# Optimization experiments

Hardware: AMD Instinct MI355X
Metric: run time of the kernel (lower is better)

Reference implementation:

```python
import jax, jax.numpy as jnp
import numpy as np
from jax import lax

# 19 edges over 19 body-joint heatmap channels (0..18); PAF channels are 19..56
EDGES = np.array([[1,8],[8,9],[9,10],[1,11],[11,12],[12,13],[1,2],[2,3],[3,4],[2,16],
                  [1,5],[5,6],[6,7],[5,17],[0,1],[0,14],[0,15],[14,16],[15,17]], dtype=np.int32)
_i = np.arange(19, dtype=np.int32)
# per-edge 4 input channels: [node_a, node_b, paf_x(=19+2i), paf_y(=20+2i)]
CH_IDX = np.concatenate([EDGES, (19 + 2*_i)[:, None], (20 + 2*_i)[:, None]], axis=1)  # [19,4]

_W_SHAPES = [(16,4,5,5),(16,16,5,5),(32,16,5,5),(32,32,5,5),(32,32,5,5),(128,32,1,1),(2,128,1,1)]

def _conv(x, w, b):
    p = (w.shape[-1] - 1) // 2  # padding=2 for 5x5, 0 for 1x1
    y = lax.conv_general_dilated(x, w, window_strides=(1,1), padding=[(p,p),(p,p)],
                                 dimension_numbers=('NCHW','OIHW','NCHW'))
    return y + b[None, :, None, None]

def setup_inputs() -> dict:
    key = jax.random.key(0)
    keys = jax.random.split(key, 1 + 2*len(_W_SHAPES))
    N, C, H, W = 16, 57, 128, 128
    inp = {'cnn_output': jax.random.normal(keys[0], (N, C, H, W), dtype=jnp.float32),
           'gnn_interations': 1}
    for i, s in enumerate(_W_SHAPES):
        inp[f'w{i}'] = jax.random.normal(keys[1+2*i], s, dtype=jnp.float32) * 0.01
        inp[f'b{i}'] = jax.random.normal(keys[2+2*i], (s[0],), dtype=jnp.float32) * 0.01
    return inp

def reference(cnn_output, gnn_interations, w0, b0, w1, b1, w2, b2, w3, b3, w4, b4, w5, b5, w6, b6):
    N, _, H, Wd = cnn_output.shape
    ws = (w0, w1, w2, w3, w4, w5, w6)
    bs = (b0, b1, b2, b3, b4, b5, b6)
    # gather per-edge 4-channel inputs: [N,19,4,H,W] -> fold edges into batch
    x = cnn_output[:, jnp.asarray(CH_IDX)]            # [N,19,4,H,W]
    x = x.reshape(N * 19, 4, H, Wd)
    for i in range(7):
        x = _conv(x, ws[i], bs[i])
        if i != 6:
            x = jax.nn.relu(x)
    # edge n output (2 ch) -> output channels [2n, 2n+1]
    return x.reshape(N, 38, H, Wd)
```

## Files before the change

kernel.cpp:

```cpp
#include <hip/hip_runtime.h>
#include <hip/hip_bf16.h>

typedef __bf16  bf16x8 __attribute__((ext_vector_type(8)));
typedef float   f32x4  __attribute__((ext_vector_type(4)));
typedef int     i32x4  __attribute__((ext_vector_type(4)));
typedef int     i32x8  __attribute__((ext_vector_type(8)));

__device__ __constant__ int EDGE_A[19] = {1,8,9,1,11,12,1,2,3,2,1,5,6,5,0,0,0,14,15};
__device__ __constant__ int EDGE_B[19] = {8,9,10,11,12,13,2,3,4,16,5,6,7,17,1,14,15,16,17};

#define SACT  64.0f
#define SINV  (1.0f / 4096.0f)
#define SREQ  0.015625f
#define SCL1  0x7F7F7F7F

__device__ __forceinline__ unsigned short f2bf(float f) {
    unsigned int x = __float_as_uint(f);
    x += 0x7FFFu + ((x >> 16) & 1u);
    return (unsigned short)(x >> 16);
}
__device__ __forceinline__ unsigned int pack2(float a, float b) {
    __hip_bfloat162 t = __float22bfloat162_rn(make_float2(a, b));
    unsigned int r; __builtin_memcpy(&r, &t, 4); return r;
}
__device__ __forceinline__ unsigned char f2fp8(float v) {
    int r = __builtin_amdgcn_cvt_pk_fp8_f32(v, 0.f, 0, false);
    return (unsigned char)(r & 0xff);
}
__device__ __forceinline__ unsigned int pk4fp8(float a, float b, float c, float d) {
    int v = __builtin_amdgcn_cvt_pk_fp8_f32(a, b, 0, false);
    v = __builtin_amdgcn_cvt_pk_fp8_f32(c, d, v, true);
    return (unsigned int)v;
}
__device__ __forceinline__ unsigned int quant4(f32x4 a, float4 b, float s, bool oob) {
    float v0 = fmaxf(fmaf(a[0], s, b.x), 0.f);
    float v1 = fmaxf(fmaf(a[1], s, b.y), 0.f);
    float v2 = fmaxf(fmaf(a[2], s, b.z), 0.f);
    float v3 = fmaxf(fmaf(a[3], s, b.w), 0.f);
    unsigned int v = pk4fp8(v0, v1, v2, v3);
    return oob ? 0u : v;
}

__device__ __forceinline__ int sw8 (int l) { return l ^ ((l >> 4) & 8);  }
__device__ __forceinline__ int sw48(int l) { return l ^ ((l >> 3) & 48); }

__device__ __forceinline__ void store_relu4(unsigned char* dst, f32x4 a, float4 b, bool oob) {
    unsigned int lo = pack2(fmaxf(a[0] + b.x, 0.f), fmaxf(a[1] + b.y, 0.f));
    unsigned int hi = pack2(fmaxf(a[2] + b.z, 0.f), fmaxf(a[3] + b.w, 0.f));
    uint2 v; v.x = oob ? 0u : lo; v.y = oob ? 0u : hi;
    *(uint2*)dst = v;
}

extern "C" __global__ void __launch_bounds__(256)
reorder_weights(const float* __restrict__ w0, const float* __restrict__ w1,
                const float* __restrict__ w2, const float* __restrict__ w3,
                const float* __restrict__ w4, const float* __restrict__ w5,
                unsigned char* __restrict__ ws)
{
    int idx = blockIdx.x * 256 + threadIdx.x;
    unsigned short* wsS = (unsigned short*)ws;
    if (idx < 4096) {
        int k = idx & 31, oc = idx >> 5;
        wsS[idx] = f2bf(w5[oc * 32 + k]);
    } else if (idx < 6144) {
        int j = idx - 4096;
        int k = j & 31, n = (j >> 5) & 15, c = j >> 9;
        int t = c * 8 + (k >> 2), ic = k & 3;
        float v = (t < 25) ? w0[(n * 4 + ic) * 25 + t] : 0.f;
        wsS[idx] = f2bf(v);
    }
    if (idx < 6656) {
        int k = idx & 31, n = (idx >> 5) & 15, tp = idx >> 9;
        int t = 2 * tp + (k >> 4), ic = k & 15;
        float v = (t < 25) ? w1[(n * 16 + ic) * 25 + t] * SACT : 0.f;
        ws[12288 + idx] = f2fp8(v);
    } else if (idx < 19968) {
        int j = idx - 6656;
        int k = j & 31, n = (j >> 5) & 15, nt = (j >> 9) & 1, tp = j >> 10;
        int t = 2 * tp + (k >> 4), ic = k & 15, oc = nt * 16 + n;
        float v = (t < 25) ? w2[(oc * 16 + ic) * 25 + t] * SACT : 0.f;
        ws[18944 + j] = f2fp8(v);
    } else if (idx < 48640) {
        int j = idx - 19968;
        int tg = j >> 12, r = j & 4095;
        int nt = r >> 11, n = (r >> 7) & 15, q = (r >> 5) & 3, ic = r & 31;
        int tap = 4 * tg + q;
        float v = (tap < 25) ? w3[((nt * 16 + n) * 32 + ic) * 25 + tap] * SACT : 0.f;
        ws[32256 + j] = f2fp8(v);
    } else if (idx < 77312) {
        int j = idx - 48640;
        int tg = j >> 12, r = j & 4095;
        int nt = r >> 11, n = (r >> 7) & 15, q = (r >> 5) & 3, ic = r & 31;
        int tap = 4 * tg + q;
        float v = (tap < 25) ? w4[((nt * 16 + n) * 32 + ic) * 25 + tap] * SACT : 0.f;
        ws[60928 + j] = f2fp8(v);
    }
}

__device__ __forceinline__ void conv0_slab(
    const unsigned short* __restrict__ s_in, unsigned char* __restrict__ s0,
    const unsigned char* __restrict__ wB, const float* __restrict__ b0,
    int yoff, int oy, int ox, int wave, int lane)
{
    const int nl = lane & 15, quad = lane >> 4;
    const unsigned short* w0p = (const unsigned short*)(wB + 8192);
    bf16x8 wf[4];
#pragma unroll
    for (int c = 0; c < 4; ++c)
        wf[c] = *(const bf16x8*)(w0p + c * 512 + nl * 32 + quad * 8);
    float4 bb = *(const float4*)(b0 + quad * 4);
    float4 bbs = make_float4(bb.x * SACT, bb.y * SACT, bb.z * SACT, bb.w * SACT);

    int coff0[4], coff1[4];
#pragma unroll
    for (int c = 0; c < 4; ++c) {
        int t0 = c * 8 + quad * 2, t1 = t0 + 1;
        if (t0 > 24) t0 = 24;
        if (t1 > 24) t1 = 24;
        coff0[c] = ((t0 / 5) * 36 + (t0 % 5)) * 8;
        coff1[c] = ((t1 / 5) * 36 + (t1 % 5)) * 8;
    }
    const unsigned char* sB = (const unsigned char*)s_in;

#pragma unroll 1
    for (int i = 0; i < 9; ++i) {
        int mt = wave + 4 * i;
        int p = mt * 16 + nl;
        int y = p >> 5, x = p & 31;
        int abase = (y * 36 + x) * 8;
        f32x4 acc = (f32x4)0.f;
#pragma unroll
        for (int c = 0; c < 4; ++c) {
            uint2 lo = *(const uint2*)(sB + abase + coff0[c]);
            uint2 hi = *(const uint2*)(sB + abase + coff1[c]);
            bf16x8 a;
            ((uint2*)&a)[0] = lo; ((uint2*)&a)[1] = hi;
            acc = __builtin_amdgcn_mfma_f32_16x16x32_bf16(wf[c], a, acc, 0, 0, 0);
        }
        bool oob = ((unsigned)(oy - 8 + y + yoff) >= 128u) || ((unsigned)(ox - 8 + x) >= 128u);
        *(unsigned int*)(s0 + sw8(p * 16 + quad * 4)) = quant4(acc, bbs, SACT, oob);
    }
}

__device__ __forceinline__ void conv1_fp8(
    const unsigned char* __restrict__ s0, unsigned char* __restrict__ s1,
    const unsigned char* __restrict__ wB, const float* __restrict__ b1,
    int POFF, int gy0, int gx0, int wave, int lane)
{
    const int nl = lane & 15, quad = lane >> 4;
    const int h = quad >> 1, g8 = (quad & 1) * 8;

    int abase[7];
#pragma unroll
    for (int i = 0; i < 7; ++i) {
        int p = (wave + 4 * i) * 16 + nl;
        if (p > 391) p = 391;
        int y = p / 28, x = p - y * 28;
        abase[i] = (y * 32 + x) * 16 + g8;
    }
    f32x4 acc[7];
#pragma unroll
    for (int i = 0; i < 7; ++i) acc[i] = (f32x4)0.f;

    const unsigned char* wp = wB + 12288 + nl * 32 + quad * 8;

#pragma unroll 1
    for (int c0 = 0; c0 < 13; c0 += 5) {
        long wl[5];
#pragma unroll
        for (int tp = 0; tp < 5; ++tp)
            if (c0 + tp < 13) wl[tp] = *(const long*)(wp + (c0 + tp) * 512);
#pragma unroll
        for (int tp = 0; tp < 5; ++tp) {
            if (c0 + tp < 13) {
                int t = 2 * (c0 + tp) + h;
                if (t > 24) t = 24;
                int dy = t / 5, dx = t - 5 * dy;
                int toff = (dy * 32 + dx) * 16;
#pragma unroll
                for (int i = 0; i < 7; ++i)
                    if (wave + 4 * i < 25) {
                        long a = *(const long*)(s0 + sw8(abase[i] + toff));
                        acc[i] = __builtin_amdgcn_mfma_f32_16x16x32_fp8_fp8(wl[tp], a, acc[i], 0, 0, 0);
                    }
            }
        }
    }

    float4 bb = *(const float4*)(b1 + quad * 4);
    float4 bbs = make_float4(bb.x * SACT, bb.y * SACT, bb.z * SACT, bb.w * SACT);
#pragma unroll
    for (int i = 0; i < 7; ++i) {
        int p = (wave + 4 * i) * 16 + nl;
        if (p < 392) {
            int pg = p + POFF;
            int y = pg / 28, x = pg - y * 28;
            bool oob = ((unsigned)(gy0 + y) >= 128u) || ((unsigned)(gx0 + x) >= 128u);
            *(unsigned int*)(s1 + sw8(pg * 16 + quad * 4)) = quant4(acc[i], bbs, SREQ, oob);
        }
    }
}

template<int I0, int NI>
__device__ __forceinline__ void conv2_fp8(
    const unsigned char* __restrict__ s1, unsigned char* __restrict__ s2,
    const unsigned char* __restrict__ wA, const float* __restrict__ b2,
    int gy0, int gx0, int wave, int lane)
{
    const int nl = lane & 15, quad = lane >> 4;
    const int h = quad >> 1, g8 = (quad & 1) * 8;

    int abase[NI];
#pragma unroll
    for (int i = 0; i < NI; ++i) {
        int p = (wave + 4 * (I0 + i)) * 16 + nl;
        int y = p / 24, x = p - y * 24;
        abase[i] = (y * 28 + x) * 16 + g8;
    }
    f32x4 acc[NI][2];
#pragma unroll
    for (int i = 0; i < NI; ++i) { acc[i][0] = (f32x4)0.f; acc[i][1] = (f32x4)0.f; }

    const unsigned char* wp = wA + nl * 32 + quad * 8;

#pragma unroll 1
    for (int c0 = 0; c0 < 13; c0 += 3) {
        long wl[3][2];
#pragma unroll
        for (int tp = 0; tp < 3; ++tp)
            if (c0 + tp < 13) {
                wl[tp][0] = *(const long*)(wp + ((c0 + tp) * 2 + 0) * 512);
                wl[tp][1] = *(const long*)(wp + ((c0 + tp) * 2 + 1) * 512);
            }
#pragma unroll
        for (int tp = 0; tp < 3; ++tp) {
            if (c0 + tp < 13) {
                int t = 2 * (c0 + tp) + h;
                if (t > 24) t = 24;
                int dy = t / 5, dx = t - 5 * dy;
                int toff = (dy * 28 + dx) * 16;
#pragma unroll
                for (int i = 0; i < NI; ++i) {
                    long a = *(const long*)(s1 + sw8(abase[i] + toff));
                    acc[i][0] = __builtin_amdgcn_mfma_f32_16x16x32_fp8_fp8(wl[tp][0], a, acc[i][0], 0, 0, 0);
                    acc[i][1] = __builtin_amdgcn_mfma_f32_16x16x32_fp8_fp8(wl[tp][1], a, acc[i][1], 0, 0, 0);
                }
            }
        }
    }

#pragma unroll
    for (int i = 0; i < NI; ++i) {
        int p = (wave + 4 * (I0 + i)) * 16 + nl;
        int y = p / 24, x = p - y * 24;
        bool oob = ((unsigned)(gy0 + y) >= 128u) || ((unsigned)(gx0 + x) >= 128u);
#pragma unroll
        for (int nt = 0; nt < 2; ++nt) {
            float4 bb = *(const float4*)(b2 + nt * 16 + quad * 4);
            float4 bbs = make_float4(bb.x * SACT, bb.y * SACT, bb.z * SACT, bb.w * SACT);
            int byte = (p * 32 + nt * 16 + quad * 4) ^ ((p & 4) << 2);
            *(unsigned int*)(s2 + byte) = quant4(acc[i][nt], bbs, SREQ, oob);
        }
    }
}

template<int SINW, int SOUT, int MAXM, bool GUARD, bool FP8OUT, bool INXOR, int INSTRIDE>
__device__ __forceinline__ void conv_c32_mx(
    const unsigned char* __restrict__ sinB, unsigned char* __restrict__ soutB,
    const unsigned char* __restrict__ wA, const float* __restrict__ bias,
    int gy0, int gx0, int wave, int lane)
{
    constexpr int NM = (SOUT * SOUT) / 16;
    const int nl = lane & 15, quad = lane >> 4;

    int abase[MAXM];
#pragma unroll
    for (int i = 0; i < MAXM; ++i) {
        int p = (wave + 4 * i) * 16 + nl;
        if (GUARD && p > SOUT * SOUT - 1) p = SOUT * SOUT - 1;
        int y = p / SOUT, x = p - y * SOUT;
        abase[i] = (y * SINW + x) * INSTRIDE;
    }
    f32x4 acc[MAXM][2];
#pragma unroll
    for (int i = 0; i < MAXM; ++i) { acc[i][0] = (f32x4)0.f; acc[i][1] = (f32x4)0.f; }

    const unsigned char* wp = wA + nl * 128 + quad * 32;

#pragma unroll 1
    for (int tg = 0; tg < 7; ++tg) {
        int t = 4 * tg + quad;
        if (t > 24) t = 24;
        int dy = t / 5, dx = t - 5 * dy;
        int to = (dy * SINW + dx) * INSTRIDE;
        i32x8 wl0 = *(const i32x8*)(wp + tg * 4096);
        i32x8 wl1 = *(const i32x8*)(wp + tg * 4096 + 2048);
#pragma unroll
        for (int i = 0; i < MAXM; ++i)
            if (!GUARD || wave + 4 * i < NM) {
                int ad = abase[i] + to;
                if (INXOR) ad ^= (ad >> 3) & 16;
                i32x4 alo = *(const i32x4*)(sinB + ad);
                i32x4 ahi = *(const i32x4*)(sinB + (INXOR ? (ad ^ 16) : (ad + 16)));
                i32x8 a;
                ((i32x4*)&a)[0] = alo; ((i32x4*)&a)[1] = ahi;
                acc[i][0] = __builtin_amdgcn_mfma_scale_f32_16x16x128_f8f6f4(
                                wl0, a, acc[i][0], 0, 0, 0, SCL1, 0, SCL1);
                acc[i][1] = __builtin_amdgcn_mfma_scale_f32_16x16x128_f8f6f4(
                                wl1, a, acc[i][1], 0, 0, 0, SCL1, 0, SCL1);
            }
    }

#pragma unroll
    for (int i = 0; i < MAXM; ++i) {
        int p = (wave + 4 * i) * 16 + nl;
        if (!GUARD || p < SOUT * SOUT) {
            int y = p / SOUT, x = p - y * SOUT;
            bool oob = ((unsigned)(gy0 + y) >= 128u) || ((unsigned)(gx0 + x) >= 128u);
#pragma unroll
            for (int nt = 0; nt < 2; ++nt) {
                float4 bb = *(const float4*)(bias + nt * 16 + quad * 4);
                if (FP8OUT) {
                    float4 bbs = make_float4(bb.x * SACT, bb.y * SACT, bb.z * SACT, bb.w * SACT);
                    *(unsigned int*)(soutB + p * 48 + nt * 16 + quad * 4) =
                        quant4(acc[i][nt], bbs, SREQ, oob);
                } else {
                    f32x4 s;
                    s[0] = acc[i][nt][0] * SINV; s[1] = acc[i][nt][1] * SINV;
                    s[2] = acc[i][nt][2] * SINV; s[3] = acc[i][nt][3] * SINV;
                    store_relu4(soutB + sw48(p * 64 + nt * 32 + quad * 8), s, bb, oob);
                }
            }
        }
    }
}

extern "C" __global__ void __launch_bounds__(256, 3)
gnn_paf_mfma(const float* __restrict__ cnn, const unsigned char* __restrict__ wB,
             const float* __restrict__ b0, const float* __restrict__ b1,
             const float* __restrict__ b2, const float* __restrict__ b3,
             const float* __restrict__ b4, const float* __restrict__ b5,
             const float* __restrict__ w6, const float* __restrict__ b6,
             float* __restrict__ out)
{
    __shared__ __align__(64) unsigned char smem[37632];
    unsigned char*  const s1   = smem;
    unsigned short* const sin_ = (unsigned short*)(smem + 12544);
    unsigned char*  const s0   = smem + 18880;
    unsigned char*  const s2   = smem + 19200;
    unsigned char*  const s3   = smem;
    unsigned char*  const s4   = smem + 19200;

    const int tid  = threadIdx.x;
    const int lane = tid & 63, wave = tid >> 6;
    const int tile = blockIdx.x, img = blockIdx.y;
    const int oy = (tile >> 3) * 16, ox = (tile & 7) * 16;
    const int n = img / 19, g = img - n * 19;
    const int ch0 = EDGE_A[g], ch1 = EDGE_B[g], ch2 = 19 + 2 * g, ch3 = 20 + 2 * g;
    const int nl = lane & 15, quad = lane >> 4;
    const long long nb = (long long)n * 57 * 16384;

    for (int idx = tid; idx < 792; idx += 256) {
        int r = idx / 36, c = idx - r * 36;
        int gy = oy - 10 + r, gx = ox - 10 + c;
        float v0 = 0.f, v1 = 0.f, v2 = 0.f, v3 = 0.f;
        if ((unsigned)gy < 128u && (unsigned)gx < 128u) {
            int off = gy * 128 + gx;
            v0 = cnn[nb + (long long)ch0 * 16384 + off];
            v1 = cnn[nb + (long long)ch1 * 16384 + off];
            v2 = cnn[nb + (long long)ch2 * 16384 + off];
            v3 = cnn[nb + (long long)ch3 * 16384 + off];
        }
        uint2 v; v.x = pack2(v0, v1); v.y = pack2(v2, v3);
        *(uint2*)(sin_ + idx * 4) = v;
    }
    __syncthreads();

    conv0_slab(sin_, s0, wB, b0, 0, oy, ox, wave, lane);
    __syncthreads();

    float gv[4][4];
#pragma unroll
    for (int j = 0; j < 4; ++j) {
        gv[j][0] = gv[j][1] = gv[j][2] = gv[j][3] = 0.f;
        int idx = tid + 256 * j;
        if (idx < 792) {
            int r = idx / 36, c = idx - r * 36;
            int gy = oy + 4 + r, gx = ox - 10 + c;
            if ((unsigned)gy < 128u && (unsigned)gx < 128u) {
                int off = gy * 128 + gx;
                gv[j][0] = cnn[nb + (long long)ch0 * 16384 + off];
                gv[j][1] = cnn[nb + (long long)ch1 * 16384 + off];
                gv[j][2] = cnn[nb + (long long)ch2 * 16384 + off];
                gv[j][3] = cnn[nb + (long long)ch3 * 16384 + off];
            }
        }
    }
    conv1_fp8(s0, s1, wB, b1, 0, oy - 6, ox - 6, wave, lane);
#pragma unroll
    for (int j = 0; j < 4; ++j) {
        int idx = tid + 256 * j;
        if (idx < 792) {
            uint2 v; v.x = pack2(gv[j][0], gv[j][1]); v.y = pack2(gv[j][2], gv[j][3]);
            *(uint2*)(sin_ + idx * 4) = v;
        }
    }
    __syncthreads();

    conv0_slab(sin_, s0, wB, b0, 14, oy, ox, wave, lane);
    __syncthreads();

    conv1_fp8(s0, s1, wB, b1, 392, oy - 6, ox - 6, wave, lane);
    __syncthreads();

    conv2_fp8<0, 5>(s1, s2, wB + 18944, b2, oy - 4, ox - 4, wave, lane);
    conv2_fp8<5, 4>(s1, s2, wB + 18944, b2, oy - 4, ox - 4, wave, lane);
    __syncthreads();

    conv_c32_mx<24, 20, 7, true,  true,  true,  32>(s2, s3, wB + 32256, b3, oy - 2, ox - 2, wave, lane);
    __syncthreads();

    conv_c32_mx<20, 16, 4, false, false, false, 48>(s3, s4, wB + 60928, b4, oy, ox, wave, lane);
    __syncthreads();

    {
        const unsigned short* w5p = (const unsigned short*)wB;
        bf16x8 w5f[8];
#pragma unroll
        for (int nt = 0; nt < 8; ++nt)
            w5f[nt] = *(const bf16x8*)(w5p + nt * 512 + nl * 32 + quad * 8);
        const float b6q = b6[quad & 1];
#pragma unroll 1
        for (int ii = 0; ii < 4; ++ii) {
            int mt = wave + 4 * ii;
            int lin = (mt * 16 + nl) * 64 + quad * 16;
            bf16x8 pf = *(const bf16x8*)(s4 + sw48(lin));
            float o0 = 0.f, o1 = 0.f;
#pragma unroll
            for (int nt = 0; nt < 8; ++nt) {
                f32x4 acc = (f32x4)0.f;
                acc = __builtin_amdgcn_mfma_f32_16x16x32_bf16(w5f[nt], pf, acc, 0, 0, 0);
                float4 bb  = *(const float4*)(b5 + nt * 16 + quad * 4);
                float4 wa  = *(const float4*)(w6 + nt * 16 + quad * 4);
                float4 wb2 = *(const float4*)(w6 + 128 + nt * 16 + quad * 4);
                float h0 = fmaxf(acc[0] + bb.x, 0.f), h1 = fmaxf(acc[1] + bb.y, 0.f);
                float h2 = fmaxf(acc[2] + bb.z, 0.f), h3 = fmaxf(acc[3] + bb.w, 0.f);
                o0 = fmaf(h0, wa.x, fmaf(h1, wa.y, fmaf(h2, wa.z, fmaf(h3, wa.w, o0))));
                o1 = fmaf(h0, wb2.x, fmaf(h1, wb2.y, fmaf(h2, wb2.z, fmaf(h3, wb2.w, o1))));
            }
            o0 += __shfl_xor(o0, 16, 64); o0 += __shfl_xor(o0, 32, 64);
            o1 += __shfl_xor(o1, 16, 64); o1 += __shfl_xor(o1, 32, 64);
            if (quad < 2) {
                float val = ((quad == 0) ? o0 : o1) + b6q;
                long long ob = (((long long)n * 38 + 2 * g + quad) * 128 + (oy + mt)) * 128 + (ox + nl);
                out[ob] = val;
            }
        }
    }
}

extern "C" void kernel_launch(void* const* d_in, const int* in_sizes, int n_in,
                              void* d_out, int out_size, void* d_ws, size_t ws_size,
                              hipStream_t stream) {
    const float* cnn = (const float*)d_in[0];
    const float* w0 = (const float*)d_in[2];  const float* b0 = (const float*)d_in[3];
    const float* w1 = (const float*)d_in[4];  const float* b1 = (const float*)d_in[5];
    const float* w2 = (const float*)d_in[6];  const float* b2 = (const float*)d_in[7];
    const float* w3 = (const float*)d_in[8];  const float* b3 = (const float*)d_in[9];
    const float* w4 = (const float*)d_in[10]; const float* b4 = (const float*)d_in[11];
    const float* w5 = (const float*)d_in[12]; const float* b5 = (const float*)d_in[13];
    const float* w6 = (const float*)d_in[14]; const float* b6 = (const float*)d_in[15];
    float* out = (float*)d_out;
    unsigned char* wB = (unsigned char*)d_ws;

    hipLaunchKernelGGL(reorder_weights, dim3(302), dim3(256), 0, stream,
                       w0, w1, w2, w3, w4, w5, wB);
    hipLaunchKernelGGL(gnn_paf_mfma, dim3(64, 304), dim3(256), 0, stream,
                       cnn, wB, b0, b1, b2, b3, b4, b5, w6, b6, out);
}
```

Measured before the change: 1.178 ms.

## Split conv1/conv3 M-tile loops into chunks and raise launch bounds to four blocks

Templates conv1_fp8 and conv_c32_mx on a starting M-tile index so each layer's seven per-wave M tiles are processed in two passes (4+3) instead of one. Fewer live accumulators per pass lower register pressure, and launch_bounds goes from 3 to 4 blocks per CU to raise occupancy. The cost is streaming weights twice per layer and losing some MFMA reuse of each weight fragment. Spills are possible if the compiler cannot fit the new register cap.

```diff
diff --git a/kernel.cpp b/kernel.cpp
--- a/kernel.cpp
+++ b/kernel.cpp
@@ -142,6 +142,7 @@
     }
 }
 
+template<int I0, int NI>
 __device__ __forceinline__ void conv1_fp8(
     const unsigned char* __restrict__ s0, unsigned char* __restrict__ s1,
     const unsigned char* __restrict__ wB, const float* __restrict__ b1,
@@ -150,17 +151,17 @@
     const int nl = lane & 15, quad = lane >> 4;
     const int h = quad >> 1, g8 = (quad & 1) * 8;
 
-    int abase[7];
-#pragma unroll
-    for (int i = 0; i < 7; ++i) {
-        int p = (wave + 4 * i) * 16 + nl;
+    int abase[NI];
+#pragma unroll
+    for (int i = 0; i < NI; ++i) {
+        int p = (wave + 4 * (I0 + i)) * 16 + nl;
         if (p > 391) p = 391;
         int y = p / 28, x = p - y * 28;
         abase[i] = (y * 32 + x) * 16 + g8;
     }
-    f32x4 acc[7];
-#pragma unroll
-    for (int i = 0; i < 7; ++i) acc[i] = (f32x4)0.f;
+    f32x4 acc[NI];
+#pragma unroll
+    for (int i = 0; i < NI; ++i) acc[i] = (f32x4)0.f;
 
     const unsigned char* wp = wB + 12288 + nl * 32 + quad * 8;
 
@@ -178,8 +179,8 @@
                 int dy = t / 5, dx = t - 5 * dy;
                 int toff = (dy * 32 + dx) * 16;
 #pragma unroll
-                for (int i = 0; i < 7; ++i)
-                    if (wave + 4 * i < 25) {
+                for (int i = 0; i < NI; ++i)
+                    if (wave + 4 * (I0 + i) < 25) {
                         long a = *(const long*)(s0 + sw8(abase[i] + toff));
                         acc[i] = __builtin_amdgcn_mfma_f32_16x16x32_fp8_fp8(wl[tp], a, acc[i], 0, 0, 0);
                     }
@@ -190,8 +191,8 @@
     float4 bb = *(const float4*)(b1 + quad * 4);
     float4 bbs = make_float4(bb.x * SACT, bb.y * SACT, bb.z * SACT, bb.w * SACT);
 #pragma unroll
-    for (int i = 0; i < 7; ++i) {
-        int p = (wave + 4 * i) * 16 + nl;
+    for (int i = 0; i < NI; ++i) {
+        int p = (wave + 4 * (I0 + i)) * 16 + nl;
         if (p < 392) {
             int pg = p + POFF;
             int y = pg / 28, x = pg - y * 28;
@@ -264,7 +265,7 @@
     }
 }
 
-template<int SINW, int SOUT, int MAXM, bool GUARD, bool FP8OUT, bool INXOR, int INSTRIDE>
+template<int SINW, int SOUT, int I0, int MAXM, bool GUARD, bool FP8OUT, bool INXOR, int INSTRIDE>
 __device__ __forceinline__ void conv_c32_mx(
     const unsigned char* __restrict__ sinB, unsigned char* __restrict__ soutB,
     const unsigned char* __restrict__ wA, const float* __restrict__ bias,
@@ -276,7 +277,7 @@
     int abase[MAXM];
 #pragma unroll
     for (int i = 0; i < MAXM; ++i) {
-        int p = (wave + 4 * i) * 16 + nl;
+        int p = (wave + 4 * (I0 + i)) * 16 + nl;
         if (GUARD && p > SOUT * SOUT - 1) p = SOUT * SOUT - 1;
         int y = p / SOUT, x = p - y * SOUT;
         abase[i] = (y * SINW + x) * INSTRIDE;
@@ -297,7 +298,7 @@
         i32x8 wl1 = *(const i32x8*)(wp + tg * 4096 + 2048);
 #pragma unroll
         for (int i = 0; i < MAXM; ++i)
-            if (!GUARD || wave + 4 * i < NM) {
+            if (!GUARD || wave + 4 * (I0 + i) < NM) {
                 int ad = abase[i] + to;
                 if (INXOR) ad ^= (ad >> 3) & 16;
                 i32x4 alo = *(const i32x4*)(sinB + ad);
@@ -313,7 +314,7 @@
 
 #pragma unroll
     for (int i = 0; i < MAXM; ++i) {
-        int p = (wave + 4 * i) * 16 + nl;
+        int p = (wave + 4 * (I0 + i)) * 16 + nl;
         if (!GUARD || p < SOUT * SOUT) {
             int y = p / SOUT, x = p - y * SOUT;
             bool oob = ((unsigned)(gy0 + y) >= 128u) || ((unsigned)(gx0 + x) >= 128u);
@@ -335,7 +336,7 @@
     }
 }
 
-extern "C" __global__ void __launch_bounds__(256, 3)
+extern "C" __global__ void __launch_bounds__(256, 4)
 gnn_paf_mfma(const float* __restrict__ cnn, const unsigned char* __restrict__ wB,
              const float* __restrict__ b0, const float* __restrict__ b1,
              const float* __restrict__ b2, const float* __restrict__ b3,
@@ -396,7 +397,8 @@
             }
         }
     }
-    conv1_fp8(s0, s1, wB, b1, 0, oy - 6, ox - 6, wave, lane);
+    conv1_fp8<0, 4>(s0, s1, wB, b1, 0, oy - 6, ox - 6, wave, lane);
+    conv1_fp8<4, 3>(s0, s1, wB, b1, 0, oy - 6, ox - 6, wave, lane);
 #pragma unroll
     for (int j = 0; j < 4; ++j) {
         int idx = tid + 256 * j;
@@ -410,17 +412,19 @@
     conv0_slab(sin_, s0, wB, b0, 14, oy, ox, wave, lane);
     __syncthreads();
 
-    conv1_fp8(s0, s1, wB, b1, 392, oy - 6, ox - 6, wave, lane);
+    conv1_fp8<0, 4>(s0, s1, wB, b1, 392, oy - 6, ox - 6, wave, lane);
+    conv1_fp8<4, 3>(s0, s1, wB, b1, 392, oy - 6, ox - 6, wave, lane);
     __syncthreads();
 
     conv2_fp8<0, 5>(s1, s2, wB + 18944, b2, oy - 4, ox - 4, wave, lane);
     conv2_fp8<5, 4>(s1, s2, wB + 18944, b2, oy - 4, ox - 4, wave, lane);
     __syncthreads();
 
-    conv_c32_mx<24, 20, 7, true,  true,  true,  32>(s2, s3, wB + 32256, b3, oy - 2, ox - 2, wave, lane);
-    __syncthreads();
-
-    conv_c32_mx<20, 16, 4, false, false, false, 48>(s3, s4, wB + 60928, b4, oy, ox, wave, lane);
+    conv_c32_mx<24, 20, 0, 4, true,  true,  true,  32>(s2, s3, wB + 32256, b3, oy - 2, ox - 2, wave, lane);
+    conv_c32_mx<24, 20, 4, 3, true,  true,  true,  32>(s2, s3, wB + 32256, b3, oy - 2, ox - 2, wave, lane);
+    __syncthreads();
+
+    conv_c32_mx<20, 16, 0, 4, false, false, false, 48>(s3, s4, wB + 60928, b4, oy, ox, wave, lane);
     __syncthreads();
 
     {
```

Result: slower. 2.054 ms (+74.4%).
